# Kernel tuning notes

Hardware: AMD Instinct MI355X
Metric: run time of the kernel (lower is better)

## Reference

```python
import jax, jax.numpy as jnp
import numpy as np

N = 98304        # total nodes (= 16384 graphs * act_dim 6)
E = 1572864      # edges (avg degree 16)
C = 64           # in_channels
H = 32           # hidden_size
ACT = 6          # act_dim


def setup_inputs() -> dict:
    key = jax.random.key(0)
    ks = jax.random.split(key, 11)
    s = lambda fan: 1.0 / np.sqrt(fan)
    return {
        "state": jax.random.normal(ks[0], (N, C), jnp.float32),
        "edge_index": jax.random.randint(ks[1], (2, E), 0, N, dtype=jnp.int64),
        "conv_W": jax.random.normal(ks[2], (C, C), jnp.float32) * s(C),
        "conv_b": jax.random.normal(ks[3], (C,), jnp.float32) * 0.01,
        "W1": jax.random.normal(ks[4], (C, H), jnp.float32) * s(C),
        "b1": jax.random.normal(ks[5], (H,), jnp.float32) * 0.01,
        "W2": jax.random.normal(ks[6], (H, H), jnp.float32) * s(H),
        "b2": jax.random.normal(ks[7], (H,), jnp.float32) * 0.01,
        "W3": jax.random.normal(ks[8], (H, 1), jnp.float32) * s(H),
        "b3": jax.random.normal(ks[9], (1,), jnp.float32) * 0.01,
    }


def gcn_conv(x, edge_index, W, b):
    # PyG GCNConv: add self-loops, symmetric normalization D^-1/2 (A+I) D^-1/2 (X W) + b
    loops = jnp.arange(N, dtype=edge_index.dtype)
    src = jnp.concatenate([edge_index[0], loops])  # [E+N]
    dst = jnp.concatenate([edge_index[1], loops])  # [E+N]
    deg = jax.ops.segment_sum(jnp.ones(E + N, x.dtype), dst, num_segments=N)
    dinv = jax.lax.rsqrt(deg)                      # deg >= 1 due to self-loops
    norm = dinv[src] * dinv[dst]                   # [E+N]
    h = x @ W                                      # [N, C]
    msg = h[src] * norm[:, None]                   # gather + scale
    return jax.ops.segment_sum(msg, dst, num_segments=N) + b


def reference(state, edge_index, conv_W, conv_b, W1, b1, W2, b2, W3, b3):
    out = jax.nn.relu(gcn_conv(state, edge_index, conv_W, conv_b))
    x = out + state                                # residual
    x = x.reshape(-1, ACT, C)                      # [num_graphs, act_dim, C]
    x = jax.nn.relu(x @ W1 + b1)
    x = jax.nn.relu(x @ W2 + b2)
    x = jax.nn.softplus(x @ W3 + b3)
    concentration = x.squeeze(-1) + 1e-20          # [num_graphs, act_dim]
    return concentration
```

## Files before the change

kernel.cpp:

```cpp
#include <hip/hip_runtime.h>
#include <math.h>

#define Nn 98304
#define Ee 1572864
#define Cc 64
#define Hh 32
#define HB 256
#define EPB (Ee / HB)
#define NST 384
#define SN 256
#define CAP_ST 4800
#define GN 64


__device__ __forceinline__ int detect64(const void* ei) {
    const unsigned int* u = (const unsigned int*)ei;
    int is64 = 1;
    #pragma unroll
    for (int i = 0; i < 16; ++i) is64 &= (u[2 * i + 1] == 0u);
    return is64;
}

__device__ __forceinline__ int load_idx(const void* ei, long e, int is64) {
    if (is64) return (int)((const long long*)ei)[e];
    return ((const int*)ei)[e];
}

__device__ __forceinline__ unsigned short f2bf(float x) {
    union { float f; unsigned int u; } v; v.f = x;
    unsigned int r = v.u + 0x7FFFu + ((v.u >> 16) & 1u);
    return (unsigned short)(r >> 16);
}
__device__ __forceinline__ float bf2f(unsigned short h) {
    union { unsigned int u; float f; } v; v.u = ((unsigned int)h) << 16;
    return v.f;
}

__device__ __forceinline__ void acc_u4(float a[8], uint4 u) {
    union { unsigned int i; float f; } w;
    w.i = u.x << 16;         a[0] += w.f;
    w.i = u.x & 0xFFFF0000u; a[1] += w.f;
    w.i = u.y << 16;         a[2] += w.f;
    w.i = u.y & 0xFFFF0000u; a[3] += w.f;
    w.i = u.z << 16;         a[4] += w.f;
    w.i = u.z & 0xFFFF0000u; a[5] += w.f;
    w.i = u.w << 16;         a[6] += w.f;
    w.i = u.w & 0xFFFF0000u; a[7] += w.f;
}
__device__ __forceinline__ void set_u4(float a[8], uint4 u) {
    union { unsigned int i; float f; } w;
    w.i = u.x << 16;         a[0] = w.f;
    w.i = u.x & 0xFFFF0000u; a[1] = w.f;
    w.i = u.y << 16;         a[2] = w.f;
    w.i = u.y & 0xFFFF0000u; a[3] = w.f;
    w.i = u.z << 16;         a[4] = w.f;
    w.i = u.z & 0xFFFF0000u; a[5] = w.f;
    w.i = u.w << 16;         a[6] = w.f;
    w.i = u.w & 0xFFFF0000u; a[7] = w.f;
}

__global__ __launch_bounds__(1024) void k_p1(const void* __restrict__ ei,
                                             unsigned int* __restrict__ aux,
                                             unsigned int* __restrict__ ebuf) {
    __shared__ unsigned int hl[NST];
    __shared__ unsigned int cur[NST];
    int t = threadIdx.x, b = blockIdx.x;
    if (t < NST) hl[t] = 0;
    __syncthreads();
    int is64 = detect64(ei);
    long e0 = (long)b * EPB;
    #pragma unroll
    for (int i = 0; i < EPB / 1024; ++i) {
        int d = load_idx(ei, (long)Ee + e0 + i * 1024 + t, is64);
        atomicAdd(&hl[d >> 8], 1u);
    }
    __syncthreads();
    if (t < NST) cur[t] = hl[t];
    __syncthreads();
    for (int s = 1; s < NST; s <<= 1) {
        unsigned int v = (t < NST && t >= s) ? cur[t - s] : 0u;
        __syncthreads();
        if (t < NST) cur[t] += v;
        __syncthreads();
    }
    if (t < NST) {
        unsigned int ex = cur[t] - hl[t];
        aux[(long)b * NST + t] = ex | (hl[t] << 16);
        cur[t] = ex;
    }
    __syncthreads();
    #pragma unroll
    for (int i = 0; i < EPB / 1024; ++i) {
        long e = e0 + i * 1024 + t;
        int s = load_idx(ei, e, is64);
        int d = load_idx(ei, (long)Ee + e, is64);
        unsigned int pos = atomicAdd(&cur[d >> 8], 1u);
        ebuf[(long)b * EPB + pos] = (unsigned int)s | ((unsigned int)(d & (SN - 1)) << 17);
    }
}

__global__ __launch_bounds__(256) void k_p2(const unsigned int* __restrict__ aux,
                                            const unsigned int* __restrict__ ebuf,
                                            unsigned int* __restrict__ rowOff,
                                            unsigned int* __restrict__ rowEnd,
                                            float* __restrict__ dinv,
                                            unsigned int* __restrict__ srcs) {
    __shared__ unsigned int stage[CAP_ST];
    __shared__ unsigned int rb[HB];
    __shared__ unsigned int cnt[SN];
    __shared__ unsigned int sc[SN];
    __shared__ unsigned int cur[SN];
    int t = threadIdx.x, st = blockIdx.x;
    unsigned int av = aux[(long)t * NST + st];
    unsigned int roff = av & 0xFFFFu, rcnt = av >> 16;
    rb[t] = rcnt;
    __syncthreads();
    for (int s = 1; s < HB; s <<= 1) {
        unsigned int v = (t >= s) ? rb[t - s] : 0u;
        __syncthreads();
        rb[t] += v;
        __syncthreads();
    }
    unsigned int mybase = rb[t] - rcnt;
    for (unsigned int i = 0; i < rcnt; ++i)
        stage[mybase + i] = ebuf[(long)t * EPB + roff + i];
    cnt[t] = 0;
    __syncthreads();
    int total = (int)rb[HB - 1];
    for (int i = t; i < total; i += 256)
        atomicAdd(&cnt[stage[i] >> 17], 1u);
    __syncthreads();
    sc[t] = cnt[t];
    __syncthreads();
    #pragma unroll
    for (int off = 1; off < SN; off <<= 1) {
        unsigned int v = (t >= off) ? sc[t - off] : 0u;
        __syncthreads();
        sc[t] += v;
        __syncthreads();
    }
    {
        unsigned int start = (unsigned int)(st * CAP_ST) + sc[t] - cnt[t];
        rowOff[(long)st * SN + t] = start;
        rowEnd[(long)st * SN + t] = start + cnt[t];
        cur[t] = start;
        dinv[(long)st * SN + t] = rsqrtf((float)(cnt[t] + 1));
    }
    __syncthreads();
    for (int i = t; i < total; i += 256) {
        unsigned int u = stage[i];
        unsigned int pos = atomicAdd(&cur[u >> 17], 1u);
        srcs[pos] = u & 0x1FFFFu;
    }
}

__global__ __launch_bounds__(256) void k_gemm(const float* __restrict__ state,
                                              const float* __restrict__ W,
                                              const float* __restrict__ dinv,
                                              unsigned short* __restrict__ gb) {
    __shared__ float Wl[64 * 64];
    __shared__ float Al[64 * 68];
    int t = threadIdx.x;
    long n0 = (long)blockIdx.x * 64;

    const float4* W4 = (const float4*)W;
    float4* Wl4 = (float4*)Wl;
    #pragma unroll
    for (int i = 0; i < 4; ++i) Wl4[i * 256 + t] = W4[i * 256 + t];

    const float4* S4 = (const float4*)(state) + n0 * 16;
    #pragma unroll
    for (int i = 0; i < 4; ++i) {
        int f4 = t + i * 256;
        int r = f4 >> 4, k0 = (f4 & 15) * 4;
        *(float4*)(Al + r * 68 + k0) = S4[f4];
    }
    __syncthreads();

    int r0 = (t >> 4) * 4;
    int c0 = (t & 15) * 4;
    float acc[4][4] = {{0.f}};
    #pragma unroll
    for (int kk = 0; kk < 64; kk += 4) {
        float4 a4[4], w4[4];
        #pragma unroll
        for (int i = 0; i < 4; ++i) a4[i] = *(const float4*)(Al + (r0 + i) * 68 + kk);
        #pragma unroll
        for (int j = 0; j < 4; ++j) w4[j] = *(const float4*)(Wl + (kk + j) * 64 + c0);
        const float* aa = (const float*)a4;
        const float* ww = (const float*)w4;
        #pragma unroll
        for (int i = 0; i < 4; ++i)
            #pragma unroll
            for (int j = 0; j < 4; ++j) {
                float av = aa[i * 4 + j];
                #pragma unroll
                for (int c = 0; c < 4; ++c)
                    acc[i][c] = fmaf(av, ww[j * 4 + c], acc[i][c]);
            }
    }
    #pragma unroll
    for (int i = 0; i < 4; ++i) {
        long n = n0 + r0 + i;
        float dv = dinv[n];
        ushort4 o;
        o.x = f2bf(acc[i][0] * dv); o.y = f2bf(acc[i][1] * dv);
        o.z = f2bf(acc[i][2] * dv); o.w = f2bf(acc[i][3] * dv);
        *(ushort4*)(gb + n * 64 + c0) = o;
    }
}

__global__ __launch_bounds__(512) void k_gf(const unsigned int* __restrict__ rowOff,
                                            const unsigned int* __restrict__ rowEnd,
                                            const unsigned int* __restrict__ srcs,
                                            const unsigned short* __restrict__ gb,
                                            const float* __restrict__ dinv,
                                            const float* __restrict__ state,
                                            const float* __restrict__ conv_b,
                                            const float* __restrict__ W1,
                                            const float* __restrict__ b1,
                                            const float* __restrict__ W2,
                                            const float* __restrict__ b2,
                                            const float* __restrict__ W3,
                                            const float* __restrict__ b3,
                                            float* __restrict__ out) {
    __shared__ float sa[GN * 68];
    __shared__ float hs[GN * 34];
    __shared__ float sW1[Cc * Hh];
    __shared__ float sW2[Hh * Hh];
    __shared__ float sW3[Hh], sb1[Hh], sb2[Hh], scb[Cc];
    __shared__ float sb3;
    int t = threadIdx.x;
    int wave = t >> 6, lane = t & 63;
    long n0 = (long)blockIdx.x * GN;

    for (int i = t; i < Cc * Hh; i += 512) sW1[i] = W1[i];
    for (int i = t; i < Hh * Hh; i += 512) sW2[i] = W2[i];
    if (t < Hh) { sW3[t] = W3[t]; sb1[t] = b1[t]; sb2[t] = b2[t]; }
    if (t >= 64 && t < 128) scb[t - 64] = conv_b[t - 64];
    if (t == 511) sb3 = b3[0];

    {
        int g = lane >> 3;
        int cs = lane & 7;
        int j = wave * 8 + g;
        long n = n0 + j;
        int ptr = (int)rowOff[n];
        int end = (int)rowEnd[n];
        float dv = dinv[n];
        const uint4* gb4 = (const uint4*)gb;

        float a[8];
        set_u4(a, gb4[n * 8 + cs]);

        int cnt = end - ptr;
        while (cnt >= 8) {
            int s0 = (int)srcs[ptr];
            int s1 = (int)srcs[ptr + 1];
            int s2 = (int)srcs[ptr + 2];
            int s3 = (int)srcs[ptr + 3];
            int s4 = (int)srcs[ptr + 4];
            int s5 = (int)srcs[ptr + 5];
            int s6 = (int)srcs[ptr + 6];
            int s7 = (int)srcs[ptr + 7];
            uint4 u0 = gb4[(long)s0 * 8 + cs];
            uint4 u1 = gb4[(long)s1 * 8 + cs];
            uint4 u2 = gb4[(long)s2 * 8 + cs];
            uint4 u3 = gb4[(long)s3 * 8 + cs];
            uint4 u4 = gb4[(long)s4 * 8 + cs];
            uint4 u5 = gb4[(long)s5 * 8 + cs];
            uint4 u6 = gb4[(long)s6 * 8 + cs];
            uint4 u7 = gb4[(long)s7 * 8 + cs];
            acc_u4(a, u0); acc_u4(a, u1); acc_u4(a, u2); acc_u4(a, u3);
            acc_u4(a, u4); acc_u4(a, u5); acc_u4(a, u6); acc_u4(a, u7);
            ptr += 8; cnt -= 8;
        }
        if (cnt >= 4) {
            int s0 = (int)srcs[ptr];
            int s1 = (int)srcs[ptr + 1];
            int s2 = (int)srcs[ptr + 2];
            int s3 = (int)srcs[ptr + 3];
            uint4 u0 = gb4[(long)s0 * 8 + cs];
            uint4 u1 = gb4[(long)s1 * 8 + cs];
            uint4 u2 = gb4[(long)s2 * 8 + cs];
            uint4 u3 = gb4[(long)s3 * 8 + cs];
            acc_u4(a, u0); acc_u4(a, u1); acc_u4(a, u2); acc_u4(a, u3);
            ptr += 4; cnt -= 4;
        }
        while (cnt > 0) {
            int s0 = (int)srcs[ptr];
            uint4 u0 = gb4[(long)s0 * 8 + cs];
            acc_u4(a, u0);
            ++ptr; --cnt;
        }

        float* r = sa + j * 68 + cs * 8;
        float4 lo, hi;
        lo.x = a[0] * dv; lo.y = a[1] * dv; lo.z = a[2] * dv; lo.w = a[3] * dv;
        hi.x = a[4] * dv; hi.y = a[5] * dv; hi.z = a[6] * dv; hi.w = a[7] * dv;
        *(float4*)r = lo;
        *(float4*)(r + 4) = hi;
    }
    __syncthreads();

    {
        int j = t >> 3, o = t & 7;
        long n = n0 + j;
        int k0 = o * 8;
        const float4* sp4 = (const float4*)(state + n * 64 + k0);
        float4 s0 = sp4[0], s1 = sp4[1];
        float* r = sa + j * 68 + k0;
        r[0] = fmaxf(r[0] + scb[k0 + 0], 0.f) + s0.x;
        r[1] = fmaxf(r[1] + scb[k0 + 1], 0.f) + s0.y;
        r[2] = fmaxf(r[2] + scb[k0 + 2], 0.f) + s0.z;
        r[3] = fmaxf(r[3] + scb[k0 + 3], 0.f) + s0.w;
        r[4] = fmaxf(r[4] + scb[k0 + 4], 0.f) + s1.x;
        r[5] = fmaxf(r[5] + scb[k0 + 5], 0.f) + s1.y;
        r[6] = fmaxf(r[6] + scb[k0 + 6], 0.f) + s1.z;
        r[7] = fmaxf(r[7] + scb[k0 + 7], 0.f) + s1.w;
    }
    __syncthreads();

    {
        int j = t >> 3, o = t & 7;
        int c0 = o * 4;
        float a0 = sb1[c0], a1 = sb1[c0 + 1], a2 = sb1[c0 + 2], a3 = sb1[c0 + 3];
        #pragma unroll
        for (int k = 0; k < Cc; ++k) {
            float xv = sa[j * 68 + k];
            float4 w = *(const float4*)(sW1 + k * Hh + c0);
            a0 = fmaf(xv, w.x, a0); a1 = fmaf(xv, w.y, a1);
            a2 = fmaf(xv, w.z, a2); a3 = fmaf(xv, w.w, a3);
        }
        float* r = hs + j * 34 + c0;
        r[0] = fmaxf(a0, 0.f); r[1] = fmaxf(a1, 0.f);
        r[2] = fmaxf(a2, 0.f); r[3] = fmaxf(a3, 0.f);
    }
    __syncthreads();

    {
        int j = t >> 3, o = t & 7;
        int c0 = o * 4;
        float a0 = sb2[c0], a1 = sb2[c0 + 1], a2 = sb2[c0 + 2], a3 = sb2[c0 + 3];
        #pragma unroll
        for (int k = 0; k < Hh; ++k) {
            float xv = hs[j * 34 + k];
            float4 w = *(const float4*)(sW2 + k * Hh + c0);
            a0 = fmaf(xv, w.x, a0); a1 = fmaf(xv, w.y, a1);
            a2 = fmaf(xv, w.z, a2); a3 = fmaf(xv, w.w, a3);
        }
        float* r = sa + j * 68 + c0;
        r[0] = fmaxf(a0, 0.f); r[1] = fmaxf(a1, 0.f);
        r[2] = fmaxf(a2, 0.f); r[3] = fmaxf(a3, 0.f);
    }
    __syncthreads();

    if (t < GN) {
        float y = sb3;
        #pragma unroll
        for (int k = 0; k < Hh; ++k) y = fmaf(sa[t * 68 + k], sW3[k], y);
        float sp = fmaxf(y, 0.f) + log1pf(expf(-fabsf(y)));
        out[n0 + t] = sp + 1e-20f;
    }
}

extern "C" void kernel_launch(void* const* d_in, const int* in_sizes, int n_in,
                              void* d_out, int out_size, void* d_ws, size_t ws_size,
                              hipStream_t stream) {
    const float* state  = (const float*)d_in[0];
    const void*  ei     = d_in[1];
    const float* conv_W = (const float*)d_in[2];
    const float* conv_b = (const float*)d_in[3];
    const float* W1 = (const float*)d_in[4];
    const float* b1 = (const float*)d_in[5];
    const float* W2 = (const float*)d_in[6];
    const float* b2 = (const float*)d_in[7];
    const float* W3 = (const float*)d_in[8];
    const float* b3 = (const float*)d_in[9];
    float* out = (float*)d_out;

    float*          dinv   = (float*)d_ws;
    unsigned short* gb     = (unsigned short*)(dinv + Nn);
    unsigned int*   rowOff = (unsigned int*)(gb + (size_t)Nn * 64);
    unsigned int*   rowEnd = rowOff + Nn;
    unsigned int*   aux    = rowEnd + Nn;
    unsigned int*   ebuf   = aux + (size_t)HB * NST;
    unsigned int*   srcs   = ebuf + Ee;

    k_p1<<<HB, 1024, 0, stream>>>(ei, aux, ebuf);
    k_p2<<<NST, 256, 0, stream>>>(aux, ebuf, rowOff, rowEnd, dinv, srcs);
    k_gemm<<<Nn / 64, 256, 0, stream>>>(state, conv_W, dinv, gb);
    k_gf<<<Nn / GN, 512, 0, stream>>>(rowOff, rowEnd, srcs, gb, dinv, state, conv_b,
                                      W1, b1, W2, b2, W3, b3, out);
}
```

Baseline: 171.5 us.

## Parallelize k_p2 staging via binary search and shrink gather unroll

The CSR-building kernel k_p2 now runs with 512 threads and fills its shared staging buffer with a flat parallel loop. Each element binary-searches the prefix-summed bucket counts to find its source block. Previously each thread serially copied one bucket's variable-length run, which gave uncoalesced, imbalanced loads. Separately, the gather loop in the fused kernel drops the 8-way unrolled body in favour of a 4-way loop with the conversion helpers inlined by hand. This probably reduces register pressure at the cost of fewer loads in flight per iteration.

Result: no change. 174.5 us (+1.7%).

```diff
diff --git a/kernel.cpp b/kernel.cpp
--- a/kernel.cpp
+++ b/kernel.cpp
@@ -36,29 +36,6 @@
     return v.f;
 }
 
-__device__ __forceinline__ void acc_u4(float a[8], uint4 u) {
-    union { unsigned int i; float f; } w;
-    w.i = u.x << 16;         a[0] += w.f;
-    w.i = u.x & 0xFFFF0000u; a[1] += w.f;
-    w.i = u.y << 16;         a[2] += w.f;
-    w.i = u.y & 0xFFFF0000u; a[3] += w.f;
-    w.i = u.z << 16;         a[4] += w.f;
-    w.i = u.z & 0xFFFF0000u; a[5] += w.f;
-    w.i = u.w << 16;         a[6] += w.f;
-    w.i = u.w & 0xFFFF0000u; a[7] += w.f;
-}
-__device__ __forceinline__ void set_u4(float a[8], uint4 u) {
-    union { unsigned int i; float f; } w;
-    w.i = u.x << 16;         a[0] = w.f;
-    w.i = u.x & 0xFFFF0000u; a[1] = w.f;
-    w.i = u.y << 16;         a[2] = w.f;
-    w.i = u.y & 0xFFFF0000u; a[3] = w.f;
-    w.i = u.z << 16;         a[4] = w.f;
-    w.i = u.z & 0xFFFF0000u; a[5] = w.f;
-    w.i = u.w << 16;         a[6] = w.f;
-    w.i = u.w & 0xFFFF0000u; a[7] = w.f;
-}
-
 __global__ __launch_bounds__(1024) void k_p1(const void* __restrict__ ei,
                                              unsigned int* __restrict__ aux,
                                              unsigned int* __restrict__ ebuf) {
@@ -99,47 +76,56 @@
     }
 }
 
-__global__ __launch_bounds__(256) void k_p2(const unsigned int* __restrict__ aux,
+__global__ __launch_bounds__(512) void k_p2(const unsigned int* __restrict__ aux,
                                             const unsigned int* __restrict__ ebuf,
                                             unsigned int* __restrict__ rowOff,
                                             unsigned int* __restrict__ rowEnd,
                                             float* __restrict__ dinv,
                                             unsigned int* __restrict__ srcs) {
     __shared__ unsigned int stage[CAP_ST];
-    __shared__ unsigned int rb[HB];
+    __shared__ unsigned int rbI[HB];
+    __shared__ unsigned int rof[HB];
     __shared__ unsigned int cnt[SN];
     __shared__ unsigned int sc[SN];
     __shared__ unsigned int cur[SN];
     int t = threadIdx.x, st = blockIdx.x;
-    unsigned int av = aux[(long)t * NST + st];
-    unsigned int roff = av & 0xFFFFu, rcnt = av >> 16;
-    rb[t] = rcnt;
+    if (t < HB) {
+        unsigned int av = aux[(long)t * NST + st];
+        rof[t] = av & 0xFFFFu;
+        rbI[t] = av >> 16;
+    }
+    if (t < SN) cnt[t] = 0;
     __syncthreads();
     for (int s = 1; s < HB; s <<= 1) {
-        unsigned int v = (t >= s) ? rb[t - s] : 0u;
-        __syncthreads();
-        rb[t] += v;
-        __syncthreads();
-    }
-    unsigned int mybase = rb[t] - rcnt;
-    for (unsigned int i = 0; i < rcnt; ++i)
-        stage[mybase + i] = ebuf[(long)t * EPB + roff + i];
-    cnt[t] = 0;
-    __syncthreads();
-    int total = (int)rb[HB - 1];
-    for (int i = t; i < total; i += 256)
+        unsigned int v = (t < HB && t >= s) ? rbI[t - s] : 0u;
+        __syncthreads();
+        if (t < HB) rbI[t] += v;
+        __syncthreads();
+    }
+    int total = (int)rbI[HB - 1];
+    for (int i = t; i < total; i += 512) {
+        int lo = 0, hi = HB - 1;
+        while (lo < hi) {
+            int mid = (lo + hi) >> 1;
+            if (rbI[mid] > (unsigned int)i) hi = mid; else lo = mid + 1;
+        }
+        unsigned int ex = lo ? rbI[lo - 1] : 0u;
+        stage[i] = ebuf[(long)lo * EPB + rof[lo] + ((unsigned int)i - ex)];
+    }
+    __syncthreads();
+    for (int i = t; i < total; i += 512)
         atomicAdd(&cnt[stage[i] >> 17], 1u);
     __syncthreads();
-    sc[t] = cnt[t];
+    if (t < SN) sc[t] = cnt[t];
     __syncthreads();
     #pragma unroll
     for (int off = 1; off < SN; off <<= 1) {
-        unsigned int v = (t >= off) ? sc[t - off] : 0u;
-        __syncthreads();
-        sc[t] += v;
-        __syncthreads();
-    }
-    {
+        unsigned int v = (t < SN && t >= off) ? sc[t - off] : 0u;
+        __syncthreads();
+        if (t < SN) sc[t] += v;
+        __syncthreads();
+    }
+    if (t < SN) {
         unsigned int start = (unsigned int)(st * CAP_ST) + sc[t] - cnt[t];
         rowOff[(long)st * SN + t] = start;
         rowEnd[(long)st * SN + t] = start + cnt[t];
@@ -147,7 +133,7 @@
         dinv[(long)st * SN + t] = rsqrtf((float)(cnt[t] + 1));
     }
     __syncthreads();
-    for (int i = t; i < total; i += 256) {
+    for (int i = t; i < total; i += 512) {
         unsigned int u = stage[i];
         unsigned int pos = atomicAdd(&cur[u >> 17], 1u);
         srcs[pos] = u & 0x1FFFFu;
@@ -251,31 +237,21 @@
         const uint4* gb4 = (const uint4*)gb;
 
         float a[8];
-        set_u4(a, gb4[n * 8 + cs]);
+        {
+            uint4 u = gb4[n * 8 + cs];
+            union { unsigned int i; float f; } w;
+            w.i = u.x << 16;         a[0] = w.f;
+            w.i = u.x & 0xFFFF0000u; a[1] = w.f;
+            w.i = u.y << 16;         a[2] = w.f;
+            w.i = u.y & 0xFFFF0000u; a[3] = w.f;
+            w.i = u.z << 16;         a[4] = w.f;
+            w.i = u.z & 0xFFFF0000u; a[5] = w.f;
+            w.i = u.w << 16;         a[6] = w.f;
+            w.i = u.w & 0xFFFF0000u; a[7] = w.f;
+        }
 
         int cnt = end - ptr;
-        while (cnt >= 8) {
-            int s0 = (int)srcs[ptr];
-            int s1 = (int)srcs[ptr + 1];
-            int s2 = (int)srcs[ptr + 2];
-            int s3 = (int)srcs[ptr + 3];
-            int s4 = (int)srcs[ptr + 4];
-            int s5 = (int)srcs[ptr + 5];
-            int s6 = (int)srcs[ptr + 6];
-            int s7 = (int)srcs[ptr + 7];
-            uint4 u0 = gb4[(long)s0 * 8 + cs];
-            uint4 u1 = gb4[(long)s1 * 8 + cs];
-            uint4 u2 = gb4[(long)s2 * 8 + cs];
-            uint4 u3 = gb4[(long)s3 * 8 + cs];
-            uint4 u4 = gb4[(long)s4 * 8 + cs];
-            uint4 u5 = gb4[(long)s5 * 8 + cs];
-            uint4 u6 = gb4[(long)s6 * 8 + cs];
-            uint4 u7 = gb4[(long)s7 * 8 + cs];
-            acc_u4(a, u0); acc_u4(a, u1); acc_u4(a, u2); acc_u4(a, u3);
-            acc_u4(a, u4); acc_u4(a, u5); acc_u4(a, u6); acc_u4(a, u7);
-            ptr += 8; cnt -= 8;
-        }
-        if (cnt >= 4) {
+        while (cnt >= 4) {
             int s0 = (int)srcs[ptr];
             int s1 = (int)srcs[ptr + 1];
             int s2 = (int)srcs[ptr + 2];
@@ -284,13 +260,53 @@
             uint4 u1 = gb4[(long)s1 * 8 + cs];
             uint4 u2 = gb4[(long)s2 * 8 + cs];
             uint4 u3 = gb4[(long)s3 * 8 + cs];
-            acc_u4(a, u0); acc_u4(a, u1); acc_u4(a, u2); acc_u4(a, u3);
+            union { unsigned int i; float f; } w;
+            w.i = u0.x << 16;         a[0] += w.f;
+            w.i = u0.x & 0xFFFF0000u; a[1] += w.f;
+            w.i = u0.y << 16;         a[2] += w.f;
+            w.i = u0.y & 0xFFFF0000u; a[3] += w.f;
+            w.i = u0.z << 16;         a[4] += w.f;
+            w.i = u0.z & 0xFFFF0000u; a[5] += w.f;
+            w.i = u0.w << 16;         a[6] += w.f;
+            w.i = u0.w & 0xFFFF0000u; a[7] += w.f;
+            w.i = u1.x << 16;         a[0] += w.f;
+            w.i = u1.x & 0xFFFF0000u; a[1] += w.f;
+            w.i = u1.y << 16;         a[2] += w.f;
+            w.i = u1.y & 0xFFFF0000u; a[3] += w.f;
+            w.i = u1.z << 16;         a[4] += w.f;
+            w.i = u1.z & 0xFFFF0000u; a[5] += w.f;
+            w.i = u1.w << 16;         a[6] += w.f;
+            w.i = u1.w & 0xFFFF0000u; a[7] += w.f;
+            w.i = u2.x << 16;         a[0] += w.f;
+            w.i = u2.x & 0xFFFF0000u; a[1] += w.f;
+            w.i = u2.y << 16;         a[2] += w.f;
+            w.i = u2.y & 0xFFFF0000u; a[3] += w.f;
+            w.i = u2.z << 16;         a[4] += w.f;
+            w.i = u2.z & 0xFFFF0000u; a[5] += w.f;
+            w.i = u2.w << 16;         a[6] += w.f;
+            w.i = u2.w & 0xFFFF0000u; a[7] += w.f;
+            w.i = u3.x << 16;         a[0] += w.f;
+            w.i = u3.x & 0xFFFF0000u; a[1] += w.f;
+            w.i = u3.y << 16;         a[2] += w.f;
+            w.i = u3.y & 0xFFFF0000u; a[3] += w.f;
+            w.i = u3.z << 16;         a[4] += w.f;
+            w.i = u3.z & 0xFFFF0000u; a[5] += w.f;
+            w.i = u3.w << 16;         a[6] += w.f;
+            w.i = u3.w & 0xFFFF0000u; a[7] += w.f;
             ptr += 4; cnt -= 4;
         }
         while (cnt > 0) {
             int s0 = (int)srcs[ptr];
             uint4 u0 = gb4[(long)s0 * 8 + cs];
-            acc_u4(a, u0);
+            union { unsigned int i; float f; } w;
+            w.i = u0.x << 16;         a[0] += w.f;
+            w.i = u0.x & 0xFFFF0000u; a[1] += w.f;
+            w.i = u0.y << 16;         a[2] += w.f;
+            w.i = u0.y & 0xFFFF0000u; a[3] += w.f;
+            w.i = u0.z << 16;         a[4] += w.f;
+            w.i = u0.z & 0xFFFF0000u; a[5] += w.f;
+            w.i = u0.w << 16;         a[6] += w.f;
+            w.i = u0.w & 0xFFFF0000u; a[7] += w.f;
             ++ptr; --cnt;
         }
 
@@ -388,7 +404,7 @@
     unsigned int*   srcs   = ebuf + Ee;
 
     k_p1<<<HB, 1024, 0, stream>>>(ei, aux, ebuf);
-    k_p2<<<NST, 256, 0, stream>>>(aux, ebuf, rowOff, rowEnd, dinv, srcs);
+    k_p2<<<NST, 512, 0, stream>>>(aux, ebuf, rowOff, rowEnd, dinv, srcs);
     k_gemm<<<Nn / 64, 256, 0, stream>>>(state, conv_W, dinv, gb);
     k_gf<<<Nn / GN, 512, 0, stream>>>(rowOff, rowEnd, srcs, gb, dinv, state, conv_b,
                                       W1, b1, W2, b2, W3, b3, out);
```
